# Kernel optimization log

Measured on AMD Instinct MI355X. Metric: run time of the kernel, lower is better.

The kernel has to match this reference:

```python
import jax, jax.numpy as jnp
import numpy as np

D, VH, DFF, NL, VOCAB, NH, NKV, HD, R, SCALE = 4096, 1024, 14336, 2, 32000, 32, 8, 128, 8, 4.0
B, NIMG, T = 2, 257, 511
S = NIMG + T

def _rmsnorm(x, w, eps=1e-5):
    v = jnp.mean(jnp.square(x), axis=-1, keepdims=True)
    return x * jax.lax.rsqrt(v + eps) * w

def _lora(x, W, A, Bm):
    # base (dequantized NF4 equivalent) matmul + low-rank LoRA path, scaling = alpha/r
    base = jnp.einsum('...d,od->...o', x, W)
    low = jnp.einsum('...r,or->...o', jnp.einsum('...d,rd->...r', x, A), Bm)
    return base + low * SCALE

def _rope_tables(s):
    inv = 1.0 / (10000.0 ** (jnp.arange(0, HD, 2, dtype=jnp.float32) / HD))
    ang = jnp.arange(s, dtype=jnp.float32)[:, None] * inv[None, :]
    c, sn = jnp.cos(ang), jnp.sin(ang)
    return jnp.concatenate([c, c], -1), jnp.concatenate([sn, sn], -1)

def _apply_rope(x, cos, sin):
    rot = jnp.concatenate([-x[..., HD // 2:], x[..., :HD // 2]], -1)
    return x * cos + rot * sin

def _forward(image_embeds, proj_W, proj_b, embed, ln1, ln2, ln_f, Wq, Aq, Bq, Wk, Ak, Bk, Wv, Av, Bv, Wo, Ao, Bo, Wg, Ag, Bg, Wu, Au, Bu, Wd, Ad, Bd, input_ids, attention_mask):
    b = image_embeds.shape[0]
    img = jnp.einsum('bsv,dv->bsd', image_embeds, proj_W) + proj_b  # projector
    txt = embed[input_ids]                                          # token embedding lookup
    h = jnp.concatenate([img, txt], axis=1)                         # (B, S, D)
    s = h.shape[1]
    cos, sin = _rope_tables(s)
    allow = jnp.tril(jnp.ones((s, s), bool))[None, None] & (attention_mask[:, None, None, :] > 0)
    for i in range(NL):
        x = _rmsnorm(h, ln1[i])
        q = _lora(x, Wq[i], Aq[i], Bq[i]).reshape(b, s, NH, HD).transpose(0, 2, 1, 3)
        k = _lora(x, Wk[i], Ak[i], Bk[i]).reshape(b, s, NKV, HD).transpose(0, 2, 1, 3)
        v = _lora(x, Wv[i], Av[i], Bv[i]).reshape(b, s, NKV, HD).transpose(0, 2, 1, 3)
        q = _apply_rope(q, cos, sin)
        k = _apply_rope(k, cos, sin)
        k = jnp.repeat(k, NH // NKV, axis=1)  # GQA: expand kv heads
        v = jnp.repeat(v, NH // NKV, axis=1)
        scores = jnp.einsum('bhsd,bhtd->bhst', q, k) / jnp.sqrt(jnp.float32(HD))
        scores = jnp.where(allow, scores, jnp.float32(-1e30))
        attn = jnp.einsum('bhst,bhtd->bhsd', jax.nn.softmax(scores, axis=-1), v)
        attn = attn.transpose(0, 2, 1, 3).reshape(b, s, D)
        h = h + _lora(attn, Wo[i], Ao[i], Bo[i])
        x = _rmsnorm(h, ln2[i])
        h = h + _lora(jax.nn.silu(_lora(x, Wg[i], Ag[i], Bg[i])) * _lora(x, Wu[i], Au[i], Bu[i]), Wd[i], Ad[i], Bd[i])
    return _rmsnorm(h, ln_f)  # HF hidden_states[-1] is post final norm

def setup_inputs():
    key = jax.random.key(0)
    ks = iter(jax.random.split(key, 40))
    n = lambda shape, sc=0.02: jax.random.normal(next(ks), shape, jnp.float32) * sc
    return dict(
        image_embeds=jax.random.normal(next(ks), (B, NIMG, VH), jnp.float32),
        input_ids=jax.random.randint(next(ks), (B, T), 0, VOCAB),
        attention_mask=jnp.ones((B, S), jnp.int32),
        proj_W=n((D, VH)), proj_b=jnp.zeros((D,), jnp.float32),
        embed=n((VOCAB, D)),
        ln1=jnp.ones((NL, D), jnp.float32), ln2=jnp.ones((NL, D), jnp.float32), ln_f=jnp.ones((D,), jnp.float32),
        Wq=n((NL, D, D)), Aq=n((NL, R, D)), Bq=n((NL, D, R)),
        Wk=n((NL, NKV * HD, D)), Ak=n((NL, R, D)), Bk=n((NL, NKV * HD, R)),
        Wv=n((NL, NKV * HD, D)), Av=n((NL, R, D)), Bv=n((NL, NKV * HD, R)),
        Wo=n((NL, D, D)), Ao=n((NL, R, D)), Bo=n((NL, D, R)),
        Wg=n((NL, DFF, D)), Ag=n((NL, R, D)), Bg=n((NL, DFF, R)),
        Wu=n((NL, DFF, D)), Au=n((NL, R, D)), Bu=n((NL, DFF, R)),
        Wd=n((NL, D, DFF)), Ad=n((NL, R, DFF)), Bd=n((NL, D, R)),
    )

def reference(image_embeds, input_ids, attention_mask, proj_W, proj_b, embed, ln1, ln2, ln_f, Wq, Aq, Bq, Wk, Ak, Bk, Wv, Av, Bv, Wo, Ao, Bo, Wg, Ag, Bg, Wu, Au, Bu, Wd, Ad, Bd):
    return _forward(image_embeds, proj_W, proj_b, embed, ln1, ln2, ln_f, Wq, Aq, Bq, Wk, Ak, Bk, Wv, Av, Bv, Wo, Ao, Bo, Wg, Ag, Bg, Wu, Au, Bu, Wd, Ad, Bd, input_ids, attention_mask)
```

## Files before the change

### kernel.cpp

```cpp
#include <hip/hip_runtime.h>
#include <hip/hip_bf16.h>
#include <cstdint>
#include <cstddef>

typedef unsigned short u16;
typedef unsigned int u32;
typedef __attribute__((ext_vector_type(8))) short short8;
typedef __attribute__((ext_vector_type(4))) short short4v;
typedef __attribute__((ext_vector_type(4))) float f32x4;

__device__ __forceinline__ u16 f2bf(float f) {
  u32 u = __float_as_uint(f);
  u32 r = (u + 0x7FFFu + ((u >> 16) & 1u)) >> 16;
  return (u16)r;
}
__device__ __forceinline__ float bf2f(u16 u) {
  return __uint_as_float(((u32)u) << 16);
}
__device__ __forceinline__ short f2bf_hw(float f) {
  union { __hip_bfloat16 h; u16 u; } c;
  c.h = __float2bfloat16(f);
  return (short)c.u;
}

__device__ __forceinline__ void gload_lds16(const void* g, void* l) {
  __builtin_amdgcn_global_load_lds((const __attribute__((address_space(1))) void*)g,
                                   (__attribute__((address_space(3))) void*)l, 16, 0, 0);
}

struct ConvJob { const float* src; u16* dst; long n8; };
struct GemmArgs {
  const u16* A; int M; int K; int lda;
  const float* W0; const float* LB0; int toff0;
  const float* W1; const float* LB1; int toff1;
  const float* W2; const float* LB2; int toff2;
  const u16* Wb0; const u16* Wb1; const u16* Wb2;
  int ldw;
  int seg1; int seg2;
  const float* t;
  const float* bias;
  const float* resid;
  float* outf; int ostride;
  u16* outb0; u16* outb1;
  int rowremap;
  float* outp;
  int ny_main;
  ConvJob cj[3];
};

template<int WMODE>
__global__ __launch_bounds__(256) void gemm_kernel(GemmArgs a) {
  __shared__ u16 Asm[128 * 64];
  __shared__ u16 BsmW[WMODE ? 128 * 64 : 128 * 128];
  const int tid = threadIdx.x;

  const int nconv = (int)gridDim.y - a.ny_main;
  if ((int)blockIdx.y < nconv) {
    if (blockIdx.z != 0) return;
    const long cb = (long)blockIdx.y * gridDim.x + blockIdx.x;
    const long cstr = (long)nconv * gridDim.x * 256;
#pragma unroll
    for (int j = 0; j < 3; j++) {
      const float* src = a.cj[j].src;
      if (!src) break;
      u16* dst = a.cj[j].dst;
      const long n8 = a.cj[j].n8;
      for (long i = cb * 256 + tid; i < n8; i += cstr) {
        const float* p = src + i * 8;
        float4 v0 = *(const float4*)p;
        float4 v1 = *(const float4*)(p + 4);
        uint4 w;
        w.x = (u32)(u16)f2bf_hw(v0.x) | ((u32)(u16)f2bf_hw(v0.y) << 16);
        w.y = (u32)(u16)f2bf_hw(v0.z) | ((u32)(u16)f2bf_hw(v0.w) << 16);
        w.z = (u32)(u16)f2bf_hw(v1.x) | ((u32)(u16)f2bf_hw(v1.y) << 16);
        w.w = (u32)(u16)f2bf_hw(v1.z) | ((u32)(u16)f2bf_hw(v1.w) << 16);
        *(uint4*)(dst + i * 8) = w;
      }
    }
    return;
  }
  const int yid = (int)blockIdx.y - nconv;

  const int nwg = gridDim.x * a.ny_main;
  const int bid0 = yid * gridDim.x + blockIdx.x;
  const int q = nwg >> 3, r = nwg & 7;
  const int xcd = bid0 & 7, pos = bid0 >> 3;
  const int nb = (xcd < r ? xcd * (q + 1) : r * (q + 1) + (xcd - r) * q) + pos;
  const int m0 = (nb % gridDim.x) * 128;
  const int n0 = (nb / gridDim.x) * 128;

  const float* W = a.W0; const u16* Wb = a.Wb0;
  const float* LB = a.LB0; int toff = a.toff0; int nbase = 0;
  if (a.seg2 && n0 >= a.seg2)      { W = a.W2; Wb = a.Wb2; LB = a.LB2; toff = a.toff2; nbase = a.seg2; }
  else if (a.seg1 && n0 >= a.seg1) { W = a.W1; Wb = a.Wb1; LB = a.LB1; toff = a.toff1; nbase = a.seg1; }
  const int koff = blockIdx.z * a.K;
  const u16* Ab = a.A + koff;
  const float* Wt = W + (size_t)(n0 - nbase) * a.ldw + koff;
  const u16* Wbt = Wb + (size_t)(n0 - nbase) * a.ldw + koff;

  const int lane = tid & 63, wid = tid >> 6;
  const int wr = wid >> 1, wcn = wid & 1;
  const int lrow = lane & 15, g = lane >> 4;
  const int arow = lane >> 3;
  const int aslot = (lane & 7) ^ arow;
  const int brow4 = lane >> 4;

  f32x4 acc[4][4] = {};

  auto dma_A = [&](int k0) {
#pragma unroll
    for (int i = 0; i < 4; i++) {
      int c = wid * 4 + i;
      const u16* src = Ab + (size_t)(m0 + c * 8 + arow) * a.lda + k0 + (aslot << 3);
      gload_lds16(src, &Asm[c * 512]);
    }
  };
  auto dma_B = [&](int k0) {
    if (WMODE) {
#pragma unroll
      for (int i = 0; i < 4; i++) {
        int c = wid * 4 + i;
        const u16* src = Wbt + (size_t)(c * 8 + arow) * a.ldw + k0 + (aslot << 3);
        gload_lds16(src, &BsmW[c * 512]);
      }
    } else {
      float* Bf = (float*)BsmW;
#pragma unroll
      for (int j = 0; j < 8; j++) {
        int rrow = wid * 32 + j * 4 + brow4;
        int sslot = (lane & 15) ^ (rrow & 7);
        const float* src = Wt + (size_t)rrow * a.ldw + k0 + (sslot << 2);
        gload_lds16(src, &Bf[(wid * 32 + j * 4) * 64]);
      }
    }
  };

  dma_A(0);
  dma_B(0);
  const int nk = a.K >> 6;
  for (int kt = 0; kt < nk; kt++) {
    __syncthreads();

    short8 af[4][2], bq[4][2];
#pragma unroll
    for (int mi = 0; mi < 4; mi++) {
      int row = wr * 64 + mi * 16 + lrow;
#pragma unroll
      for (int x = 0; x < 2; x++) {
        int s = x * 4 + g;
        af[mi][x] = *(const short8*)&Asm[row * 64 + ((s ^ (lrow & 7)) << 3)];
      }
    }
#pragma unroll
    for (int ni = 0; ni < 4; ni++) {
      int row = wcn * 64 + ni * 16 + lrow;
      if (WMODE) {
#pragma unroll
        for (int x = 0; x < 2; x++) {
          int s = x * 4 + g;
          bq[ni][x] = *(const short8*)&BsmW[row * 64 + ((s ^ (lrow & 7)) << 3)];
        }
      } else {
        const float* bp = (const float*)BsmW + row * 64;
        int m = row & 7;
#pragma unroll
        for (int x = 0; x < 2; x++) {
          int sg0 = x * 8 + g * 2;
          f32x4 lo = *(const f32x4*)(bp + ((sg0 ^ m) << 2));
          f32x4 hi = *(const f32x4*)(bp + (((sg0 + 1) ^ m) << 2));
          short8 sv;
          sv[0] = f2bf_hw(lo[0]); sv[1] = f2bf_hw(lo[1]);
          sv[2] = f2bf_hw(lo[2]); sv[3] = f2bf_hw(lo[3]);
          sv[4] = f2bf_hw(hi[0]); sv[5] = f2bf_hw(hi[1]);
          sv[6] = f2bf_hw(hi[2]); sv[7] = f2bf_hw(hi[3]);
          bq[ni][x] = sv;
        }
      }
    }

    asm volatile("s_waitcnt lgkmcnt(0)" ::: "memory");
    __builtin_amdgcn_sched_barrier(0);
    __builtin_amdgcn_s_barrier();
    __builtin_amdgcn_sched_barrier(0);
    if (kt + 1 < nk) {
      dma_A((kt + 1) << 6);
      dma_B((kt + 1) << 6);
    }
#pragma unroll
    for (int x = 0; x < 2; x++)
#pragma unroll
      for (int mi = 0; mi < 4; mi++)
#pragma unroll
        for (int ni = 0; ni < 4; ni++)
          acc[mi][ni] = __builtin_amdgcn_mfma_f32_16x16x32_bf16(af[mi][x], bq[ni][x], acc[mi][ni], 0, 0, 0);
  }

  if (a.outp) {
    float* op = a.outp + (size_t)blockIdx.z * (1536 * 4096);
#pragma unroll
    for (int mi = 0; mi < 4; mi++)
#pragma unroll
      for (int rr = 0; rr < 4; rr++) {
        int row = m0 + wr * 64 + mi * 16 + (g << 2) + rr;
#pragma unroll
        for (int ni = 0; ni < 4; ni++) {
          int n = n0 + wcn * 64 + ni * 16 + lrow;
          op[(size_t)row * a.ostride + n] = acc[mi][ni][rr];
        }
      }
    return;
  }
  const bool dolora = (a.t != nullptr);
  float lbv[4][8];
#pragma unroll
  for (int ni = 0; ni < 4; ni++) {
    if (dolora) {
      int cl = wcn * 64 + ni * 16 + lrow;
      const float* bp = LB + (size_t)(n0 - nbase + cl) * 8;
#pragma unroll
      for (int r2 = 0; r2 < 8; r2++) lbv[ni][r2] = bp[r2];
    }
  }
#pragma unroll
  for (int mi = 0; mi < 4; mi++) {
#pragma unroll
    for (int rr = 0; rr < 4; rr++) {
      int row = m0 + wr * 64 + mi * 16 + (g << 2) + rr;
      if (row >= a.M) continue;
      float tv[8];
      if (dolora) {
        const float* tp = a.t + row * 32 + toff;
#pragma unroll
        for (int r2 = 0; r2 < 8; r2++) tv[r2] = tp[r2];
      }
#pragma unroll
      for (int ni = 0; ni < 4; ni++) {
        int n = n0 + wcn * 64 + ni * 16 + lrow;
        float val = acc[mi][ni][rr];
        if (dolora) {
          float ds = 0.f;
#pragma unroll
          for (int r2 = 0; r2 < 8; r2++) ds += tv[r2] * lbv[ni][r2];
          val += 4.0f * ds;
        }
        if (a.bias)  val += a.bias[n];
        if (a.resid) val += a.resid[(size_t)row * 4096 + n];
        if (a.outf) {
          int orow = a.rowremap ? (row < 257 ? row : row + 511) : row;
          a.outf[(size_t)orow * a.ostride + n] = val;
        } else if (a.seg1 && n >= a.seg1) {
          a.outb1[(size_t)row * a.ostride + (n - a.seg1)] = f2bf(val);
        } else {
          a.outb0[(size_t)row * a.ostride + n] = f2bf(val);
        }
      }
    }
  }
}

__global__ __launch_bounds__(256) void combine_kernel(float* __restrict__ h,
    const float* __restrict__ p, const float* __restrict__ t,
    const float* __restrict__ LB) {
  const int row = blockIdx.x;
  float tv[8];
  const float* tp = t + row * 32;
#pragma unroll
  for (int r = 0; r < 8; r++) tv[r] = tp[r];
  const float* p1 = p + (size_t)1536 * 4096;
#pragma unroll
  for (int i = 0; i < 4; i++) {
    int base = threadIdx.x * 4 + i * 1024;
    size_t off = (size_t)row * 4096 + base;
    float4 hv = *(const float4*)(h + off);
    float4 a0 = *(const float4*)(p + off);
    float4 a1 = *(const float4*)(p1 + off);
    float o[4] = {hv.x + a0.x + a1.x, hv.y + a0.y + a1.y,
                  hv.z + a0.z + a1.z, hv.w + a0.w + a1.w};
#pragma unroll
    for (int j = 0; j < 4; j++) {
      const float* lb = LB + (size_t)(base + j) * 8;
      float ds = 0.f;
#pragma unroll
      for (int r = 0; r < 8; r++) ds += tv[r] * lb[r];
      o[j] += 4.0f * ds;
    }
    float4 ov; ov.x = o[0]; ov.y = o[1]; ov.z = o[2]; ov.w = o[3];
    *(float4*)(h + off) = ov;
  }
}

template<int NA>
__global__ __launch_bounds__(256) void lora_xa_kernel(const u16* __restrict__ X, int K,
    const float* A0, const float* A1, const float* A2, float* __restrict__ t) {
  const int m = blockIdx.x;
  const u16* xr = X + (size_t)m * K;
  float acc[NA * 8];
#pragma unroll
  for (int i = 0; i < NA * 8; i++) acc[i] = 0.f;
  const float* Ap[3] = {A0, A1, A2};
  for (int k = threadIdx.x * 8; k < K; k += 2048) {
    uint4 xv = *(const uint4*)(xr + k);
    float xf[8];
    xf[0] = bf2f((u16)(xv.x & 0xffff)); xf[1] = bf2f((u16)(xv.x >> 16));
    xf[2] = bf2f((u16)(xv.y & 0xffff)); xf[3] = bf2f((u16)(xv.y >> 16));
    xf[4] = bf2f((u16)(xv.z & 0xffff)); xf[5] = bf2f((u16)(xv.z >> 16));
    xf[6] = bf2f((u16)(xv.w & 0xffff)); xf[7] = bf2f((u16)(xv.w >> 16));
#pragma unroll
    for (int aa = 0; aa < NA; aa++) {
#pragma unroll
      for (int r = 0; r < 8; r++) {
        const float* ar = Ap[aa] + (size_t)r * K + k;
        float4 a0 = *(const float4*)ar;
        float4 a1 = *(const float4*)(ar + 4);
        acc[aa * 8 + r] += xf[0] * a0.x + xf[1] * a0.y + xf[2] * a0.z + xf[3] * a0.w
                         + xf[4] * a1.x + xf[5] * a1.y + xf[6] * a1.z + xf[7] * a1.w;
      }
    }
  }
  __shared__ float red[4][NA * 8];
#pragma unroll
  for (int i = 0; i < NA * 8; i++) {
    float v = acc[i];
#pragma unroll
    for (int o = 1; o < 64; o <<= 1) v += __shfl_xor(v, o);
    if ((threadIdx.x & 63) == 0) red[threadIdx.x >> 6][i] = v;
  }
  __syncthreads();
  if (threadIdx.x < NA * 8)
    t[m * 32 + threadIdx.x] = red[0][threadIdx.x] + red[1][threadIdx.x]
                            + red[2][threadIdx.x] + red[3][threadIdx.x];
}

__global__ __launch_bounds__(256) void rmsnorm_kernel(const float* __restrict__ h,
    const float* __restrict__ w, u16* outb, float* outf) {
  const int m = blockIdx.x;
  const float* row = h + (size_t)m * 4096;
  float4 v[4];
  float ss = 0.f;
#pragma unroll
  for (int i = 0; i < 4; i++) {
    v[i] = *(const float4*)(row + threadIdx.x * 4 + i * 1024);
    ss += v[i].x * v[i].x + v[i].y * v[i].y + v[i].z * v[i].z + v[i].w * v[i].w;
  }
#pragma unroll
  for (int o = 1; o < 64; o <<= 1) ss += __shfl_xor(ss, o);
  __shared__ float red[4];
  if ((threadIdx.x & 63) == 0) red[threadIdx.x >> 6] = ss;
  __syncthreads();
  ss = red[0] + red[1] + red[2] + red[3];
  float rs = rsqrtf(ss * (1.f / 4096.f) + 1e-5f);
#pragma unroll
  for (int i = 0; i < 4; i++) {
    int base = threadIdx.x * 4 + i * 1024;
    float4 wv = *(const float4*)(w + base);
    float o0 = v[i].x * rs * wv.x, o1 = v[i].y * rs * wv.y;
    float o2 = v[i].z * rs * wv.z, o3 = v[i].w * rs * wv.w;
    if (outb) {
      short4v sv; sv.x = (short)f2bf(o0); sv.y = (short)f2bf(o1);
      sv.z = (short)f2bf(o2); sv.w = (short)f2bf(o3);
      *(short4v*)(outb + (size_t)m * 4096 + base) = sv;
    } else {
      float4 ov; ov.x = o0; ov.y = o1; ov.z = o2; ov.w = o3;
      *(float4*)(outf + (size_t)m * 4096 + base) = ov;
    }
  }
}

__global__ void rope_tab_kernel(float2* __restrict__ tab) {
  int idx = blockIdx.x * 256 + threadIdx.x;
  int s = idx >> 6, i = idx & 63;
  float inv = __expf(-(float)i * (9.210340371976184f / 64.f));
  float ang = (float)s * inv;
  float sn, cs;
  sincosf(ang, &sn, &cs);
  float2 r; r.x = cs; r.y = sn;
  tab[idx] = r;
}

__global__ __launch_bounds__(256) void rope_apply_kernel(float* __restrict__ qkv,
    const float2* __restrict__ tab) {
  int m = blockIdx.x;
  int s = m % 768;
  float* rowp = qkv + (size_t)m * 6144;
  for (int idx = threadIdx.x; idx < 2560; idx += 256) {
    int head = idx >> 6, i = idx & 63;
    int col = (head < 32) ? head * 128 : 4096 + (head - 32) * 128;
    float2 cs = tab[s * 64 + i];
    float x0 = rowp[col + i], x1 = rowp[col + i + 64];
    rowp[col + i]      = x0 * cs.x - x1 * cs.y;
    rowp[col + i + 64] = x1 * cs.x + x0 * cs.y;
  }
}

__global__ __launch_bounds__(256) void attn_mfma_kernel(const float* __restrict__ qkv,
    const int* __restrict__ amask, u16* __restrict__ attn_bf) {
  __shared__ u16 Ks[4][32][40];
  __shared__ u16 Vt[128][40];
  __shared__ u16 Ps[4][16][40];
  const int b = blockIdx.z, hh = blockIdx.y, q0 = blockIdx.x * 64;
  const int kvh = hh >> 2;
  const int tid = threadIdx.x, lane = tid & 63, w = tid >> 6;
  const int lrow = lane & 15, g = lane >> 4;
  const float sc = 0.08838834764831845f;

  short8 qf[4];
  {
    const float* qp = qkv + ((size_t)(b * 768 + q0 + w * 16 + lrow)) * 6144 + hh * 128;
#pragma unroll
    for (int ks = 0; ks < 4; ks++) {
      float4 lo = *(const float4*)(qp + ks * 32 + g * 8);
      float4 hi = *(const float4*)(qp + ks * 32 + g * 8 + 4);
      short8 sv;
      sv[0] = f2bf_hw(lo.x * sc); sv[1] = f2bf_hw(lo.y * sc);
      sv[2] = f2bf_hw(lo.z * sc); sv[3] = f2bf_hw(lo.w * sc);
      sv[4] = f2bf_hw(hi.x * sc); sv[5] = f2bf_hw(hi.y * sc);
      sv[6] = f2bf_hw(hi.z * sc); sv[7] = f2bf_hw(hi.w * sc);
      qf[ks] = sv;
    }
  }

  f32x4 acco[8] = {};
  float mrun[4] = {-1e30f, -1e30f, -1e30f, -1e30f};
  float lrun[4] = {0.f, 0.f, 0.f, 0.f};
  const int ntile = (q0 >> 5) + 2;

  for (int kt = 0; kt < ntile; kt++) {
    const int k0 = kt * 32;
    __syncthreads();
#pragma unroll
    for (int i = 0; i < 4; i++) {
      int idx = i * 256 + tid;
      int r2 = idx >> 5, c4 = (idx & 31) << 2;
      const float* kp = qkv + ((size_t)(b * 768 + k0 + r2)) * 6144 + 4096 + kvh * 128 + c4;
      float4 kv = *(const float4*)kp;
      short4v ksv;
      ksv.x = f2bf_hw(kv.x); ksv.y = f2bf_hw(kv.y);
      ksv.z = f2bf_hw(kv.z); ksv.w = f2bf_hw(kv.w);
      *(short4v*)&Ks[c4 >> 5][r2][c4 & 31] = ksv;
      float4 vv = *(const float4*)(kp + 1024);
      Vt[c4 + 0][r2] = (u16)f2bf_hw(vv.x);
      Vt[c4 + 1][r2] = (u16)f2bf_hw(vv.y);
      Vt[c4 + 2][r2] = (u16)f2bf_hw(vv.z);
      Vt[c4 + 3][r2] = (u16)f2bf_hw(vv.w);
    }
    __syncthreads();

    f32x4 s0 = {}, s1 = {};
#pragma unroll
    for (int ks = 0; ks < 4; ks++) {
      short8 kb0 = *(const short8*)&Ks[ks][lrow][g * 8];
      short8 kb1 = *(const short8*)&Ks[ks][16 + lrow][g * 8];
      s0 = __builtin_amdgcn_mfma_f32_16x16x32_bf16(qf[ks], kb0, s0, 0, 0, 0);
      s1 = __builtin_amdgcn_mfma_f32_16x16x32_bf16(qf[ks], kb1, s1, 0, 0, 0);
    }
    const int key0 = k0 + lrow, key1 = k0 + 16 + lrow;
    const bool am0 = amask[b * 768 + key0] != 0;
    const bool am1 = amask[b * 768 + key1] != 0;
    float scl4[4];
#pragma unroll
    for (int rr = 0; rr < 4; rr++) {
      int qrow = q0 + w * 16 + g * 4 + rr;
      float v0 = (key0 <= qrow && am0) ? s0[rr] : -1e30f;
      float v1 = (key1 <= qrow && am1) ? s1[rr] : -1e30f;
      float m = fmaxf(v0, v1);
      m = fmaxf(m, __shfl_xor(m, 1));
      m = fmaxf(m, __shfl_xor(m, 2));
      m = fmaxf(m, __shfl_xor(m, 4));
      m = fmaxf(m, __shfl_xor(m, 8));
      float mnew = fmaxf(mrun[rr], m);
      float scl = __expf(mrun[rr] - mnew);
      float p0 = __expf(v0 - mnew);
      float p1 = __expf(v1 - mnew);
      float ls = p0 + p1;
      ls += __shfl_xor(ls, 1);
      ls += __shfl_xor(ls, 2);
      ls += __shfl_xor(ls, 4);
      ls += __shfl_xor(ls, 8);
      lrun[rr] = lrun[rr] * scl + ls;
      mrun[rr] = mnew;
      scl4[rr] = scl;
      Ps[w][g * 4 + rr][lrow]      = (u16)f2bf_hw(p0);
      Ps[w][g * 4 + rr][16 + lrow] = (u16)f2bf_hw(p1);
    }
#pragma unroll
    for (int nf = 0; nf < 8; nf++)
#pragma unroll
      for (int rr = 0; rr < 4; rr++) acco[nf][rr] *= scl4[rr];

    asm volatile("s_waitcnt lgkmcnt(0)" ::: "memory");
    __builtin_amdgcn_sched_barrier(0);
    short8 pa = *(const short8*)&Ps[w][lrow][g * 8];
#pragma unroll
    for (int nf = 0; nf < 8; nf++) {
      short8 vb = *(const short8*)&Vt[nf * 16 + lrow][g * 8];
      acco[nf] = __builtin_amdgcn_mfma_f32_16x16x32_bf16(pa, vb, acco[nf], 0, 0, 0);
    }
  }

#pragma unroll
  for (int rr = 0; rr < 4; rr++) {
    float inv = 1.f / lrun[rr];
    size_t orow = (size_t)(b * 768 + q0 + w * 16 + g * 4 + rr);
#pragma unroll
    for (int nf = 0; nf < 8; nf++)
      attn_bf[orow * 4096 + hh * 128 + nf * 16 + lrow] = f2bf(acco[nf][rr] * inv);
  }
}

__global__ void convert_img_kernel(const float* __restrict__ in, u16* __restrict__ out) {
  int idx = blockIdx.x * 256 + threadIdx.x;
  if (idx >= 81920) return;
  uint4 w = {0u, 0u, 0u, 0u};
  if (idx < 65792) {
    const float* p = in + (size_t)idx * 8;
    float4 v0 = *(const float4*)p;
    float4 v1 = *(const float4*)(p + 4);
    w.x = (u32)f2bf(v0.x) | ((u32)f2bf(v0.y) << 16);
    w.y = (u32)f2bf(v0.z) | ((u32)f2bf(v0.w) << 16);
    w.z = (u32)f2bf(v1.x) | ((u32)f2bf(v1.y) << 16);
    w.w = (u32)f2bf(v1.z) | ((u32)f2bf(v1.w) << 16);
  }
  *(uint4*)(out + (size_t)idx * 8) = w;
}

__global__ void embed_gather_kernel(const float* __restrict__ embed,
    const int* __restrict__ ids, float* __restrict__ h) {
  int row = blockIdx.x;
  int b = row / 511, tt = row % 511;
  int id = ids[b * 511 + tt];
  const float* src = embed + (size_t)id * 4096;
  float* dst = h + ((size_t)(b * 768 + 257 + tt)) * 4096;
  for (int i = threadIdx.x * 4; i < 4096; i += 1024)
    *(float4*)(dst + i) = *(const float4*)(src + i);
}

__global__ __launch_bounds__(256) void gu_combine_kernel(const u16* __restrict__ g,
    const u16* __restrict__ u, u16* __restrict__ x2) {
  size_t idx = (size_t)blockIdx.x * 256 + threadIdx.x;
  uint4 gv = *(const uint4*)(g + idx * 8);
  uint4 uv = *(const uint4*)(u + idx * 8);
  u32 gi[4] = {gv.x, gv.y, gv.z, gv.w};
  u32 ui[4] = {uv.x, uv.y, uv.z, uv.w};
  u32 oi[4];
#pragma unroll
  for (int i = 0; i < 4; i++) {
    float g0 = bf2f((u16)(gi[i] & 0xffff)), g1 = bf2f((u16)(gi[i] >> 16));
    float u0 = bf2f((u16)(ui[i] & 0xffff)), u1 = bf2f((u16)(ui[i] >> 16));
    float s0 = g0 / (1.f + __expf(-g0)) * u0;
    float s1 = g1 / (1.f + __expf(-g1)) * u1;
    oi[i] = (u32)f2bf(s0) | ((u32)f2bf(s1) << 16);
  }
  uint4 ov; ov.x = oi[0]; ov.y = oi[1]; ov.z = oi[2]; ov.w = oi[3];
  *(uint4*)(x2 + idx * 8) = ov;
}

extern "C" void kernel_launch(void* const* d_in, const int* in_sizes, int n_in,
                              void* d_out, int out_size, void* d_ws, size_t ws_size,
                              hipStream_t stream) {
  const float* image_embeds = (const float*)d_in[0];
  const int*   input_ids    = (const int*)d_in[1];
  const int*   amask        = (const int*)d_in[2];
  const float* proj_W = (const float*)d_in[3];
  const float* proj_b = (const float*)d_in[4];
  const float* embed  = (const float*)d_in[5];
  const float* ln1 = (const float*)d_in[6];
  const float* ln2 = (const float*)d_in[7];
  const float* ln_f = (const float*)d_in[8];
  const float* Wq = (const float*)d_in[9];
  const float* Aq = (const float*)d_in[10];
  const float* Bq = (const float*)d_in[11];
  const float* Wk = (const float*)d_in[12];
  const float* Ak = (const float*)d_in[13];
  const float* Bk = (const float*)d_in[14];
  const float* Wv = (const float*)d_in[15];
  const float* Av = (const float*)d_in[16];
  const float* Bv = (const float*)d_in[17];
  const float* Wo = (const float*)d_in[18];
  const float* Ao = (const float*)d_in[19];
  const float* Bo = (const float*)d_in[20];
  const float* Wg = (const float*)d_in[21];
  const float* Ag = (const float*)d_in[22];
  const float* Bg = (const float*)d_in[23];
  const float* Wu = (const float*)d_in[24];
  const float* Au = (const float*)d_in[25];
  const float* Bu = (const float*)d_in[26];
  const float* Wd = (const float*)d_in[27];
  const float* Ad = (const float*)d_in[28];
  const float* Bd = (const float*)d_in[29];
  (void)in_sizes; (void)n_in; (void)out_size;

  char* ws = (char*)d_ws;
  size_t off = 0;
  auto alloc = [&](size_t bytes) -> void* {
    void* p = ws + off; off += (bytes + 255) & ~(size_t)255; return p;
  };
  float* h       = (float*) alloc((size_t)1536 * 4096 * 4);
  u16*   xn      = (u16*)   alloc((size_t)1536 * 4096 * 2);
  float* qkv     = (float*) alloc((size_t)1536 * 6144 * 4);
  u16*   attn_bf = (u16*)   alloc((size_t)1536 * 4096 * 2);
  u16*   g_bf    = (u16*)   alloc((size_t)1536 * 14336 * 2);
  u16*   u_bf    = (u16*)   alloc((size_t)1536 * 14336 * 2);
  u16*   x2_bf   = (u16*)   alloc((size_t)1536 * 14336 * 2);
  float* t       = (float*) alloc((size_t)1536 * 32 * 4);
  float2* tab    = (float2*)alloc((size_t)768 * 64 * 8);
  u16*   img_bf  = (u16*)   alloc((size_t)640 * 1024 * 2);
  float* pc      = (float*) alloc((size_t)2 * 1536 * 4096 * 4);
  const size_t nQ = (size_t)2 * 4096 * 4096;
  const size_t nK = (size_t)2 * 1024 * 4096;
  const size_t nG = (size_t)2 * 14336 * 4096;
  const long nQl8 = 4096L * 4096 / 8, nKl8 = 1024L * 4096 / 8, nGl8 = 14336L * 4096 / 8;
  u16* wq_b = (u16*)alloc(nQ * 2);
  u16* wk_b = (u16*)alloc(nK * 2);
  u16* wv_b = (u16*)alloc(nK * 2);
  u16* wo_b = (u16*)alloc(nQ * 2);
  u16* wg_b = (u16*)alloc(nG * 2);
  u16* wu_b = (u16*)alloc(nG * 2);
  u16* wd_b = (u16*)alloc(nG * 2);
  const bool use_bf = (off <= ws_size);
  const int CONVY = 16;

  dim3 blk(256);
  auto launch_gemm = [&](const GemmArgs& a, dim3 grid) {
    if (a.Wb0) gemm_kernel<1><<<grid, blk, 0, stream>>>(a);
    else       gemm_kernel<0><<<grid, blk, 0, stream>>>(a);
  };

  convert_img_kernel<<<dim3(320), blk, 0, stream>>>(image_embeds, img_bf);
  rope_tab_kernel<<<dim3(192), blk, 0, stream>>>(tab);

  {
    GemmArgs a = {};
    a.A = img_bf; a.M = 514; a.K = 1024; a.lda = 1024; a.ldw = 1024;
    a.W0 = proj_W;
    a.bias = proj_b;
    a.outf = h; a.ostride = 4096; a.rowremap = 1;
    a.ny_main = 32;
    dim3 grid(5, 32);
    if (use_bf) {
      a.cj[0] = {Wq, wq_b, nQl8};
      a.cj[1] = {Wk, wk_b, nKl8};
      a.cj[2] = {Wv, wv_b, nKl8};
      grid = dim3(5, 32 + 2 * CONVY);
    }
    launch_gemm(a, grid);
  }
  embed_gather_kernel<<<dim3(1022), blk, 0, stream>>>(embed, input_ids, h);

  for (int l = 0; l < 2; l++) {
    const float* Wq_l = Wq + (size_t)l * 4096 * 4096;
    const float* Aq_l = Aq + (size_t)l * 8 * 4096;
    const float* Bq_l = Bq + (size_t)l * 4096 * 8;
    const float* Wk_l = Wk + (size_t)l * 1024 * 4096;
    const float* Ak_l = Ak + (size_t)l * 8 * 4096;
    const float* Bk_l = Bk + (size_t)l * 1024 * 8;
    const float* Wv_l = Wv + (size_t)l * 1024 * 4096;
    const float* Av_l = Av + (size_t)l * 8 * 4096;
    const float* Bv_l = Bv + (size_t)l * 1024 * 8;
    const float* Wo_l = Wo + (size_t)l * 4096 * 4096;
    const float* Ao_l = Ao + (size_t)l * 8 * 4096;
    const float* Bo_l = Bo + (size_t)l * 4096 * 8;
    const float* Wg_l = Wg + (size_t)l * 14336 * 4096;
    const float* Ag_l = Ag + (size_t)l * 8 * 4096;
    const float* Bg_l = Bg + (size_t)l * 14336 * 8;
    const float* Wu_l = Wu + (size_t)l * 14336 * 4096;
    const float* Au_l = Au + (size_t)l * 8 * 4096;
    const float* Bu_l = Bu + (size_t)l * 14336 * 8;
    const float* Wd_l = Wd + (size_t)l * 4096 * 14336;
    const float* Ad_l = Ad + (size_t)l * 8 * 14336;
    const float* Bd_l = Bd + (size_t)l * 4096 * 8;
    u16* wq_bl = wq_b + (size_t)l * 4096 * 4096;
    u16* wk_bl = wk_b + (size_t)l * 1024 * 4096;
    u16* wv_bl = wv_b + (size_t)l * 1024 * 4096;
    u16* wo_bl = wo_b + (size_t)l * 4096 * 4096;
    u16* wg_bl = wg_b + (size_t)l * 14336 * 4096;
    u16* wu_bl = wu_b + (size_t)l * 14336 * 4096;
    u16* wd_bl = wd_b + (size_t)l * 14336 * 4096;

    rmsnorm_kernel<<<dim3(1536), blk, 0, stream>>>(h, ln1 + l * 4096, xn, (float*)nullptr);
    lora_xa_kernel<3><<<dim3(1536), blk, 0, stream>>>(xn, 4096, Aq_l, Ak_l, Av_l, t);
    {
      GemmArgs a = {};
      a.A = xn; a.M = 1536; a.K = 4096; a.lda = 4096; a.ldw = 4096;
      a.W0 = Wq_l; a.LB0 = Bq_l; a.toff0 = 0;
      a.W1 = Wk_l; a.LB1 = Bk_l; a.toff1 = 8;
      a.W2 = Wv_l; a.LB2 = Bv_l; a.toff2 = 16;
      a.seg1 = 4096; a.seg2 = 5120;
      a.t = t; a.outf = qkv; a.ostride = 6144;
      a.ny_main = 48;
      dim3 grid(12, 48);
      if (use_bf) {
        a.Wb0 = wq_bl; a.Wb1 = wk_bl; a.Wb2 = wv_bl;
        a.cj[0] = {Wo_l, wo_bl, nQl8};
        a.cj[1] = {Wg_l, wg_bl, nGl8};
        grid = dim3(12, 48 + CONVY);
      }
      launch_gemm(a, grid);
    }
    rope_apply_kernel<<<dim3(1536), blk, 0, stream>>>(qkv, tab);
    attn_mfma_kernel<<<dim3(12, 32, 2), blk, 0, stream>>>(qkv, amask, attn_bf);
    lora_xa_kernel<1><<<dim3(1536), blk, 0, stream>>>(attn_bf, 4096, Ao_l,
        (const float*)nullptr, (const float*)nullptr, t);
    {
      GemmArgs a = {};
      a.A = attn_bf; a.M = 1536; a.K = 2048; a.lda = 4096; a.ldw = 4096;
      a.W0 = Wo_l;
      a.ostride = 4096; a.outp = pc;
      a.ny_main = 32;
      dim3 grid(12, 32, 2);
      if (use_bf) {
        a.Wb0 = wo_bl;
        a.cj[0] = {Wu_l, wu_bl, nGl8};
        grid = dim3(12, 32 + CONVY, 2);
      }
      launch_gemm(a, grid);
      combine_kernel<<<dim3(1536), blk, 0, stream>>>(h, pc, t, Bo_l);
    }
    rmsnorm_kernel<<<dim3(1536), blk, 0, stream>>>(h, ln2 + l * 4096, xn, (float*)nullptr);
    lora_xa_kernel<2><<<dim3(1536), blk, 0, stream>>>(xn, 4096, Ag_l, Au_l,
        (const float*)nullptr, t);
    {
      GemmArgs a = {};
      a.A = xn; a.M = 1536; a.K = 4096; a.lda = 4096; a.ldw = 4096;
      a.W0 = Wg_l; a.LB0 = Bg_l; a.toff0 = 0;
      a.W1 = Wu_l; a.LB1 = Bu_l; a.toff1 = 8;
      a.seg1 = 14336;
      a.t = t; a.outb0 = g_bf; a.outb1 = u_bf; a.ostride = 14336;
      a.ny_main = 224;
      dim3 grid(12, 224);
      if (use_bf) {
        a.Wb0 = wg_bl; a.Wb1 = wu_bl;
        a.cj[0] = {Wd_l, wd_bl, nGl8};
        grid = dim3(12, 224 + CONVY);
      }
      launch_gemm(a, grid);
    }
    gu_combine_kernel<<<dim3(10752), blk, 0, stream>>>(g_bf, u_bf, x2_bf);
    lora_xa_kernel<1><<<dim3(1536), blk, 0, stream>>>(x2_bf, 14336, Ad_l,
        (const float*)nullptr, (const float*)nullptr, t);
    {
      GemmArgs a = {};
      a.A = x2_bf; a.M = 1536; a.K = 7168; a.lda = 14336; a.ldw = 14336;
      a.W0 = Wd_l;
      a.ostride = 4096; a.outp = pc;
      a.ny_main = 32;
      dim3 grid(12, 32, 2);
      if (use_bf) {
        a.Wb0 = wd_bl;
        if (l == 0) {
          a.cj[0] = {Wq + (size_t)4096 * 4096, wq_b + (size_t)4096 * 4096, nQl8};
          a.cj[1] = {Wk + (size_t)1024 * 4096, wk_b + (size_t)1024 * 4096, nKl8};
          a.cj[2] = {Wv + (size_t)1024 * 4096, wv_b + (size_t)1024 * 4096, nKl8};
          grid = dim3(12, 32 + CONVY, 2);
        }
      }
      launch_gemm(a, grid);
      combine_kernel<<<dim3(1536), blk, 0, stream>>>(h, pc, t, Bd_l);
    }
  }
  rmsnorm_kernel<<<dim3(1536), blk, 0, stream>>>(h, ln_f, (u16*)nullptr, (float*)d_out);
}
```

Baseline: 3.034 ms.

## Fuse RoPE into attention loads and SwiGLU combine into LoRA down-projection

RoPE is no longer a separate in-place pass over qkv. The attention kernel now applies the rotation while loading Q fragments and K tiles, reading the paired half-dimension and the cos/sin table directly. The gate/up SiLU combine is merged with the LoRA x·A reduction for the down projection, so x2 is computed and reduced in one kernel instead of being written and then re-read. This removes two launches and several full-activation round trips, at the cost of redundant RoPE work on K, which is recomputed for every query block and head sharing a KV head.

```diff
diff --git a/kernel.cpp b/kernel.cpp
--- a/kernel.cpp
+++ b/kernel.cpp
@@ -331,6 +331,55 @@
                             + red[2][threadIdx.x] + red[3][threadIdx.x];
 }
 
+__global__ __launch_bounds__(256) void gu_lora_kernel(const u16* __restrict__ g,
+    const u16* __restrict__ u, u16* __restrict__ x2,
+    const float* __restrict__ Ad, float* __restrict__ t) {
+  const int m = blockIdx.x, tid = threadIdx.x;
+  float acc[8];
+#pragma unroll
+  for (int r = 0; r < 8; r++) acc[r] = 0.f;
+  const size_t rb = (size_t)m * 14336;
+  for (int k = tid * 8; k < 14336; k += 2048) {
+    uint4 gv = *(const uint4*)(g + rb + k);
+    uint4 uv = *(const uint4*)(u + rb + k);
+    u32 gi[4] = {gv.x, gv.y, gv.z, gv.w};
+    u32 ui[4] = {uv.x, uv.y, uv.z, uv.w};
+    u32 oi[4];
+    float xf[8];
+#pragma unroll
+    for (int i = 0; i < 4; i++) {
+      float g0 = bf2f((u16)(gi[i] & 0xffff)), g1 = bf2f((u16)(gi[i] >> 16));
+      float u0 = bf2f((u16)(ui[i] & 0xffff)), u1 = bf2f((u16)(ui[i] >> 16));
+      float s0 = g0 / (1.f + __expf(-g0)) * u0;
+      float s1 = g1 / (1.f + __expf(-g1)) * u1;
+      u16 b0 = f2bf(s0), b1 = f2bf(s1);
+      oi[i] = (u32)b0 | ((u32)b1 << 16);
+      xf[2 * i] = bf2f(b0); xf[2 * i + 1] = bf2f(b1);
+    }
+    uint4 ov; ov.x = oi[0]; ov.y = oi[1]; ov.z = oi[2]; ov.w = oi[3];
+    *(uint4*)(x2 + rb + k) = ov;
+#pragma unroll
+    for (int r = 0; r < 8; r++) {
+      const float* ar = Ad + (size_t)r * 14336 + k;
+      float4 a0 = *(const float4*)ar;
+      float4 a1 = *(const float4*)(ar + 4);
+      acc[r] += xf[0] * a0.x + xf[1] * a0.y + xf[2] * a0.z + xf[3] * a0.w
+              + xf[4] * a1.x + xf[5] * a1.y + xf[6] * a1.z + xf[7] * a1.w;
+    }
+  }
+  __shared__ float red[4][8];
+#pragma unroll
+  for (int i = 0; i < 8; i++) {
+    float v = acc[i];
+#pragma unroll
+    for (int o = 1; o < 64; o <<= 1) v += __shfl_xor(v, o);
+    if ((tid & 63) == 0) red[tid >> 6][i] = v;
+  }
+  __syncthreads();
+  if (tid < 8)
+    t[m * 32 + tid] = red[0][tid] + red[1][tid] + red[2][tid] + red[3][tid];
+}
+
 __global__ __launch_bounds__(256) void rmsnorm_kernel(const float* __restrict__ h,
     const float* __restrict__ w, u16* outb, float* outf) {
   const int m = blockIdx.x;
@@ -377,23 +426,9 @@
   tab[idx] = r;
 }
 
-__global__ __launch_bounds__(256) void rope_apply_kernel(float* __restrict__ qkv,
-    const float2* __restrict__ tab) {
-  int m = blockIdx.x;
-  int s = m % 768;
-  float* rowp = qkv + (size_t)m * 6144;
-  for (int idx = threadIdx.x; idx < 2560; idx += 256) {
-    int head = idx >> 6, i = idx & 63;
-    int col = (head < 32) ? head * 128 : 4096 + (head - 32) * 128;
-    float2 cs = tab[s * 64 + i];
-    float x0 = rowp[col + i], x1 = rowp[col + i + 64];
-    rowp[col + i]      = x0 * cs.x - x1 * cs.y;
-    rowp[col + i + 64] = x1 * cs.x + x0 * cs.y;
-  }
-}
-
 __global__ __launch_bounds__(256) void attn_mfma_kernel(const float* __restrict__ qkv,
-    const int* __restrict__ amask, u16* __restrict__ attn_bf) {
+    const int* __restrict__ amask, const float2* __restrict__ tab,
+    u16* __restrict__ attn_bf) {
   __shared__ u16 Ks[4][32][40];
   __shared__ u16 Vt[128][40];
   __shared__ u16 Ps[4][16][40];
@@ -403,19 +438,27 @@
   const int lrow = lane & 15, g = lane >> 4;
   const float sc = 0.08838834764831845f;
 
+  const int spos = q0 + w * 16 + lrow;
   short8 qf[4];
   {
-    const float* qp = qkv + ((size_t)(b * 768 + q0 + w * 16 + lrow)) * 6144 + hh * 128;
-#pragma unroll
-    for (int ks = 0; ks < 4; ks++) {
-      float4 lo = *(const float4*)(qp + ks * 32 + g * 8);
-      float4 hi = *(const float4*)(qp + ks * 32 + g * 8 + 4);
-      short8 sv;
-      sv[0] = f2bf_hw(lo.x * sc); sv[1] = f2bf_hw(lo.y * sc);
-      sv[2] = f2bf_hw(lo.z * sc); sv[3] = f2bf_hw(lo.w * sc);
-      sv[4] = f2bf_hw(hi.x * sc); sv[5] = f2bf_hw(hi.y * sc);
-      sv[6] = f2bf_hw(hi.z * sc); sv[7] = f2bf_hw(hi.w * sc);
-      qf[ks] = sv;
+    const float* qp = qkv + ((size_t)(b * 768 + spos)) * 6144 + hh * 128;
+#pragma unroll
+    for (int ks = 0; ks < 2; ks++) {
+      int c0 = ks * 32 + g * 8;
+      float4 lo  = *(const float4*)(qp + c0);
+      float4 hi  = *(const float4*)(qp + c0 + 4);
+      float4 plo = *(const float4*)(qp + c0 + 64);
+      float4 phi = *(const float4*)(qp + c0 + 68);
+      float x[8] = {lo.x, lo.y, lo.z, lo.w, hi.x, hi.y, hi.z, hi.w};
+      float p[8] = {plo.x, plo.y, plo.z, plo.w, phi.x, phi.y, phi.z, phi.w};
+      short8 aa, bb;
+#pragma unroll
+      for (int j = 0; j < 8; j++) {
+        float2 cs = tab[spos * 64 + c0 + j];
+        aa[j] = f2bf_hw((x[j] * cs.x - p[j] * cs.y) * sc);
+        bb[j] = f2bf_hw((p[j] * cs.x + x[j] * cs.y) * sc);
+      }
+      qf[ks] = aa; qf[ks + 2] = bb;
     }
   }
 
@@ -431,13 +474,22 @@
     for (int i = 0; i < 4; i++) {
       int idx = i * 256 + tid;
       int r2 = idx >> 5, c4 = (idx & 31) << 2;
-      const float* kp = qkv + ((size_t)(b * 768 + k0 + r2)) * 6144 + 4096 + kvh * 128 + c4;
-      float4 kv = *(const float4*)kp;
+      const float* kbase = qkv + ((size_t)(b * 768 + k0 + r2)) * 6144 + 4096 + kvh * 128;
+      float4 kv = *(const float4*)(kbase + c4);
+      float4 pv = *(const float4*)(kbase + (c4 ^ 64));
+      int ci = c4 & 63;
+      float2 t0 = tab[(k0 + r2) * 64 + ci];
+      float2 t1 = tab[(k0 + r2) * 64 + ci + 1];
+      float2 t2 = tab[(k0 + r2) * 64 + ci + 2];
+      float2 t3 = tab[(k0 + r2) * 64 + ci + 3];
+      float sgn = (c4 < 64) ? -1.f : 1.f;
       short4v ksv;
-      ksv.x = f2bf_hw(kv.x); ksv.y = f2bf_hw(kv.y);
-      ksv.z = f2bf_hw(kv.z); ksv.w = f2bf_hw(kv.w);
+      ksv.x = f2bf_hw(kv.x * t0.x + sgn * (pv.x * t0.y));
+      ksv.y = f2bf_hw(kv.y * t1.x + sgn * (pv.y * t1.y));
+      ksv.z = f2bf_hw(kv.z * t2.x + sgn * (pv.z * t2.y));
+      ksv.w = f2bf_hw(kv.w * t3.x + sgn * (pv.w * t3.y));
       *(short4v*)&Ks[c4 >> 5][r2][c4 & 31] = ksv;
-      float4 vv = *(const float4*)(kp + 1024);
+      float4 vv = *(const float4*)(kbase + 1024 + c4);
       Vt[c4 + 0][r2] = (u16)f2bf_hw(vv.x);
       Vt[c4 + 1][r2] = (u16)f2bf_hw(vv.y);
       Vt[c4 + 2][r2] = (u16)f2bf_hw(vv.z);
@@ -532,26 +584,6 @@
   float* dst = h + ((size_t)(b * 768 + 257 + tt)) * 4096;
   for (int i = threadIdx.x * 4; i < 4096; i += 1024)
     *(float4*)(dst + i) = *(const float4*)(src + i);
-}
-
-__global__ __launch_bounds__(256) void gu_combine_kernel(const u16* __restrict__ g,
-    const u16* __restrict__ u, u16* __restrict__ x2) {
-  size_t idx = (size_t)blockIdx.x * 256 + threadIdx.x;
-  uint4 gv = *(const uint4*)(g + idx * 8);
-  uint4 uv = *(const uint4*)(u + idx * 8);
-  u32 gi[4] = {gv.x, gv.y, gv.z, gv.w};
-  u32 ui[4] = {uv.x, uv.y, uv.z, uv.w};
-  u32 oi[4];
-#pragma unroll
-  for (int i = 0; i < 4; i++) {
-    float g0 = bf2f((u16)(gi[i] & 0xffff)), g1 = bf2f((u16)(gi[i] >> 16));
-    float u0 = bf2f((u16)(ui[i] & 0xffff)), u1 = bf2f((u16)(ui[i] >> 16));
-    float s0 = g0 / (1.f + __expf(-g0)) * u0;
-    float s1 = g1 / (1.f + __expf(-g1)) * u1;
-    oi[i] = (u32)f2bf(s0) | ((u32)f2bf(s1) << 16);
-  }
-  uint4 ov; ov.x = oi[0]; ov.y = oi[1]; ov.z = oi[2]; ov.w = oi[3];
-  *(uint4*)(x2 + idx * 8) = ov;
 }
 
 extern "C" void kernel_launch(void* const* d_in, const int* in_sizes, int n_in,
@@ -696,8 +728,7 @@
       }
       launch_gemm(a, grid);
     }
-    rope_apply_kernel<<<dim3(1536), blk, 0, stream>>>(qkv, tab);
-    attn_mfma_kernel<<<dim3(12, 32, 2), blk, 0, stream>>>(qkv, amask, attn_bf);
+    attn_mfma_kernel<<<dim3(12, 32, 2), blk, 0, stream>>>(qkv, amask, tab, attn_bf);
     lora_xa_kernel<1><<<dim3(1536), blk, 0, stream>>>(attn_bf, 4096, Ao_l,
         (const float*)nullptr, (const float*)nullptr, t);
     {
@@ -734,9 +765,7 @@
       }
       launch_gemm(a, grid);
     }
-    gu_combine_kernel<<<dim3(10752), blk, 0, stream>>>(g_bf, u_bf, x2_bf);
-    lora_xa_kernel<1><<<dim3(1536), blk, 0, stream>>>(x2_bf, 14336, Ad_l,
-        (const float*)nullptr, (const float*)nullptr, t);
+    gu_lora_kernel<<<dim3(1536), blk, 0, stream>>>(g_bf, u_bf, x2_bf, Ad_l, t);
     {
       GemmArgs a = {};
       a.A = x2_bf; a.M = 1536; a.K = 7168; a.lda = 14336; a.ldw = 14336;
```

Result: no change. 3.056 ms (+0.7%).
